# Kernel tuning notes

Measured on AMD Instinct MI355X. Metric: run time of the kernel, lower is better.

The kernel has to match this reference:

```python
import jax, jax.numpy as jnp
import numpy as np

EMBED_DIM = 1024
NUM_HEADS = 8
SEQ_LEN = 2048
EPS = 1e-6


def setup_inputs() -> dict:
    key = jax.random.key(0)
    ks = jax.random.split(key, 8)
    E, NH, S = EMBED_DIM, NUM_HEADS, SEQ_LEN
    q = jax.random.normal(ks[0], (S, E), jnp.float32)
    k = jax.random.normal(ks[1], (S, E), jnp.float32)
    v = jax.random.normal(ks[2], (S, E), jnp.float32)
    # gate projections: weights init'd to zeros in the module; use small random
    # values so the gate math is exercised. Biases follow the module's init.
    Wi = 0.02 * jax.random.normal(ks[3], (NH, 3 * E), jnp.float32)
    bi = jnp.linspace(3.0, 6.0, NH, dtype=jnp.float32)
    Wf = 0.02 * jax.random.normal(ks[4], (NH, 3 * E), jnp.float32)
    bf = jnp.sqrt(0.1) * jax.random.normal(ks[5], (NH,), jnp.float32)
    # ResidualLayerNorm (xLSTM-style): effective scale = 1 + weight, no bias
    ln_weight = jnp.zeros((E,), jnp.float32)
    return {"q": q, "k": k, "v": v, "Wi": Wi, "bi": bi, "Wf": Wf, "bf": bf,
            "ln_weight": ln_weight}


def _mlstm_parallel(q, k, v, Wi, bi, Wf, bf, ln_weight):
    S, E = q.shape
    NH = Wi.shape[0]
    DH = E // NH
    gate_in = jnp.concatenate((q, k, v), axis=1)            # (S, 3E)
    ig = (gate_in @ Wi.T + bi).T[:, :, None]                # (NH, S, 1)
    fg = (gate_in @ Wf.T + bf).T[:, :, None]                # (NH, S, 1)

    qh = q.reshape(S, NH, DH).transpose(1, 0, 2)            # (NH, S, DH)
    kh = k.reshape(S, NH, DH).transpose(1, 0, 2)
    vh = v.reshape(S, NH, DH).transpose(1, 0, 2)

    # cumulative log forget gates
    log_f = jax.nn.log_sigmoid(fg)                          # (NH, S, 1)
    log_f_cum = jnp.concatenate(
        [jnp.zeros((NH, 1, 1), q.dtype), jnp.cumsum(log_f, axis=1)], axis=1
    )                                                       # (NH, S+1, 1)
    log_fg_mat = log_f_cum - log_f_cum.transpose(0, 2, 1)   # (NH, S+1, S+1)
    causal = jnp.tril(jnp.ones((S, S), bool))
    log_fg_mat = jnp.where(causal, log_fg_mat[:, 1:, 1:], -jnp.inf)  # (NH,S,S)

    log_D = log_fg_mat + ig.transpose(0, 2, 1)              # (NH, S, S)
    max_log_D = jnp.max(log_D, axis=-1, keepdims=True)      # (NH, S, 1)
    D = jnp.exp(log_D - max_log_D)                          # stabilized

    qk = jnp.einsum('hsd,htd->hst', qh, kh) / jnp.sqrt(jnp.asarray(DH, q.dtype))
    C = qk * D                                              # (NH, S, S)
    normalizer = jnp.maximum(jnp.abs(jnp.sum(C, axis=-1, keepdims=True)),
                             jnp.exp(-max_log_D))
    C_norm = C / (normalizer + EPS)
    h = jnp.einsum('hst,htd->hsd', C_norm, vh)              # (NH, S, DH)
    h = h.transpose(1, 0, 2).reshape(S, E)

    # residual layer norm: LN(h) * (1 + weight), no bias
    mu = jnp.mean(h, axis=-1, keepdims=True)
    var = jnp.mean(jnp.square(h - mu), axis=-1, keepdims=True)
    h_norm = (h - mu) * jax.lax.rsqrt(var + 1e-5)
    return h_norm * (1.0 + ln_weight)


def reference(q, k, v, Wi, bi, Wf, bf, ln_weight):
    return _mlstm_parallel(q, k, v, Wi, bi, Wf, bf, ln_weight)
```

## Files before the change

kernel.cpp:

```cpp
#include <hip/hip_runtime.h>
#include <math.h>

#define S_LEN 2048
#define EMB   1024
#define NHEAD 8
#define DH    128
#define E3    3072
#define BM    64
#define BN    32
#define NSPLIT 4
#define KSTRIDE  136
#define VTSTRIDE 40
#define PTSTRIDE 40

typedef __bf16 bf16x8 __attribute__((ext_vector_type(8)));
typedef __bf16 bf16x4 __attribute__((ext_vector_type(4)));
typedef float  f32x4  __attribute__((ext_vector_type(4)));

__global__ __launch_bounds__(256) void gates_cvt_transpose_kernel(
    const float* __restrict__ q, const float* __restrict__ k,
    const float* __restrict__ v,
    const float* __restrict__ Wi, const float* __restrict__ bi,
    const float* __restrict__ Wf, const float* __restrict__ bf,
    __bf16* __restrict__ Qh, __bf16* __restrict__ Ql,
    __bf16* __restrict__ Kh, __bf16* __restrict__ Kl,
    __bf16* __restrict__ Vt,
    float* __restrict__ ig, float* __restrict__ lf)
{
    const int tid = threadIdx.x;
    __shared__ union {
        float red[16][4];
        __bf16 tile[32][33];
    } sh;

    if (blockIdx.x < S_LEN) {
        const int t = blockIdx.x;
        const float4 qv = ((const float4*)q)[(size_t)t * 256 + tid];
        const float4 kv = ((const float4*)k)[(size_t)t * 256 + tid];
        const float4 vv = ((const float4*)v)[(size_t)t * 256 + tid];
        {
            size_t idx = (size_t)t * 256 + tid;
            bf16x4 hi, lo;
            hi[0]=(__bf16)qv.x; hi[1]=(__bf16)qv.y; hi[2]=(__bf16)qv.z; hi[3]=(__bf16)qv.w;
            lo[0]=(__bf16)(qv.x-(float)hi[0]); lo[1]=(__bf16)(qv.y-(float)hi[1]);
            lo[2]=(__bf16)(qv.z-(float)hi[2]); lo[3]=(__bf16)(qv.w-(float)hi[3]);
            ((bf16x4*)Qh)[idx] = hi; ((bf16x4*)Ql)[idx] = lo;
            hi[0]=(__bf16)kv.x; hi[1]=(__bf16)kv.y; hi[2]=(__bf16)kv.z; hi[3]=(__bf16)kv.w;
            lo[0]=(__bf16)(kv.x-(float)hi[0]); lo[1]=(__bf16)(kv.y-(float)hi[1]);
            lo[2]=(__bf16)(kv.z-(float)hi[2]); lo[3]=(__bf16)(kv.w-(float)hi[3]);
            ((bf16x4*)Kh)[idx] = hi; ((bf16x4*)Kl)[idx] = lo;
        }
        float acc[16];
        #pragma unroll
        for (int g = 0; g < 16; ++g) {
            const float4* w4 = (const float4*)((g < 8) ? (Wi + g * E3) : (Wf + (g - 8) * E3));
            float4 a = w4[tid], b = w4[256 + tid], c = w4[512 + tid];
            acc[g] = a.x*qv.x + a.y*qv.y + a.z*qv.z + a.w*qv.w
                   + b.x*kv.x + b.y*kv.y + b.z*kv.z + b.w*kv.w
                   + c.x*vv.x + c.y*vv.y + c.z*vv.z + c.w*vv.w;
        }
        const int w = tid >> 6, lane = tid & 63;
        #pragma unroll
        for (int g = 0; g < 16; ++g) {
            float x = acc[g];
            for (int o = 32; o > 0; o >>= 1) x += __shfl_down(x, o, 64);
            if (lane == 0) sh.red[g][w] = x;
        }
        __syncthreads();
        if (tid < 16) {
            float s = sh.red[tid][0] + sh.red[tid][1] + sh.red[tid][2] + sh.red[tid][3];
            if (tid < 8) {
                ig[tid * S_LEN + t] = s + bi[tid];
            } else {
                int h = tid - 8;
                float x = s + bf[h];
                lf[h * S_LEN + t] = fminf(x, 0.f) - log1pf(expf(-fabsf(x)));
            }
        }
    } else {
        const int tb = blockIdx.x - S_LEN;
        const int sb = (tb & 63) * 32, eb = (tb >> 6) * 32;
        #pragma unroll
        for (int i = 0; i < 4; ++i) {
            int lin = tid + i * 256;
            int sr = lin >> 5, ec = lin & 31;
            sh.tile[ec][sr] = (__bf16)v[(size_t)(sb + sr) * EMB + eb + ec];
        }
        __syncthreads();
        #pragma unroll
        for (int i = 0; i < 4; ++i) {
            int lin = tid + i * 256;
            int er = lin >> 5, sc = lin & 31;
            Vt[(size_t)(eb + er) * S_LEN + sb + sc] = sh.tile[er][sc];
        }
    }
}

__global__ __launch_bounds__(256) void cumsum_aux_kernel(
    const float* __restrict__ lf, const float* __restrict__ ig,
    float* __restrict__ F, float* __restrict__ ug,
    float* __restrict__ umax, float* __restrict__ upmax)
{
    const int h = blockIdx.x, tid = threadIdx.x;
    __shared__ float ssum[256];
    __shared__ float morig[256];
    float loc[8];
    const int base = tid * 8;
    float s = 0.f;
    for (int i = 0; i < 8; i++) { s += lf[h * S_LEN + base + i]; loc[i] = s; }
    ssum[tid] = s;
    __syncthreads();
    for (int o = 1; o < 256; o <<= 1) {
        float add = (tid >= o) ? ssum[tid - o] : 0.f;
        __syncthreads();
        ssum[tid] += add;
        __syncthreads();
    }
    float prev = (tid > 0) ? ssum[tid - 1] : 0.f;
    float* Fh = F + h * (S_LEN + 1);
    if (tid == 0) Fh[0] = 0.f;
    float Fv[8];
    for (int i = 0; i < 8; i++) { Fv[i] = prev + loc[i]; Fh[base + i + 1] = Fv[i]; }

    const float* igh = ig + h * S_LEN;
    float pm[8];
    float runm = -1e30f;
    #pragma unroll
    for (int i = 0; i < 8; i++) {
        float u = igh[base + i] - Fv[i];
        ug[h * S_LEN + base + i] = u;
        runm = fmaxf(runm, u);
        pm[i] = runm;
    }
    morig[tid] = runm;
    __syncthreads();
    const int g0 = tid & ~3;
    float pfx = -1e30f;
    for (int j = g0; j < tid; ++j) pfx = fmaxf(pfx, morig[j]);
    #pragma unroll
    for (int i = 0; i < 8; i++)
        upmax[h * S_LEN + base + i] = fmaxf(pfx, pm[i]);
    if ((tid & 3) == 0) {
        float mm = fmaxf(fmaxf(morig[tid], morig[tid + 1]),
                         fmaxf(morig[tid + 2], morig[tid + 3]));
        umax[h * 64 + (tid >> 2)] = mm;
    }
}

__global__ __launch_bounds__(256, 2) void mlstm_mfma(
    const __bf16* __restrict__ Qhg, const __bf16* __restrict__ Qlg,
    const __bf16* __restrict__ Khg, const __bf16* __restrict__ Klg,
    const __bf16* __restrict__ Vtg,
    const float* __restrict__ ug, const float* __restrict__ umaxg,
    const float* __restrict__ upmaxg, const float* __restrict__ F,
    __bf16* __restrict__ Opart, float* __restrict__ msplit,
    float* __restrict__ lsplit)
{
    const int flat = blockIdx.x;
    const int h = flat & 7;
    const int rest = flat >> 3;
    const int xx = rest & 15, z = rest >> 4;
    const int tid  = threadIdx.x;
    const int lane = tid & 63, w = tid >> 6;
    const int quad = lane >> 4, l15 = lane & 15;

    __shared__ __bf16 Kh[BN * KSTRIDE], Kl[BN * KSTRIDE];
    __shared__ __bf16 Vt[DH * VTSTRIDE];
    __shared__ __bf16 Pt[4][16 * PTSTRIDE];

    const float* Fh  = F  + h * (S_LEN + 1);
    const float* ugh = ug + h * S_LEN;
    const float scale = 0.088388347648318447f;
    const int kr  = tid >> 4, kc8 = tid & 15;
    const int vr0 = tid >> 2, vc0 = tid & 3;

    for (int pair = 0; pair < 2; ++pair) {
        const int qt = (pair == 0) ? xx : 31 - xx;
        const int qb = qt * BM;
        const int nj = 2 * qt + 2;
        const int j0 = (z * nj) / NSPLIT, j1 = ((z + 1) * nj) / NSPLIT;

        float fq[4], upm[4];
        int sglob[4], sblk[4];
        #pragma unroll
        for (int r = 0; r < 4; ++r) {
            int s = qb + w * 16 + quad * 4 + r;
            sglob[r] = s; sblk[r] = s >> 5;
            fq[r]  = Fh[s + 1];
            upm[r] = upmaxg[h * S_LEN + s];
        }
        float m_r[4] = {-1e30f, -1e30f, -1e30f, -1e30f};
        float l_r[4] = {0.f, 0.f, 0.f, 0.f};
        f32x4 Oacc[8] = {{0,0,0,0},{0,0,0,0},{0,0,0,0},{0,0,0,0},
                         {0,0,0,0},{0,0,0,0},{0,0,0,0},{0,0,0,0}};

        bf16x8 pk[2], pl[2], pv[2];
        if (j0 < j1) {
            const int tb = j0 * BN;
            #pragma unroll
            for (int i = 0; i < 2; ++i) {
                int row = kr + 16 * i;
                size_t g = (size_t)(tb + row) * EMB + h * DH + kc8 * 8;
                pk[i] = *(const bf16x8*)(Khg + g);
                pl[i] = *(const bf16x8*)(Klg + g);
                pv[i] = *(const bf16x8*)(Vtg + (size_t)(h * DH + vr0 + 64 * i) * S_LEN + tb + vc0 * 8);
            }
        }

        for (int j = j0; j < j1; ++j) {
            const int tb = j * BN;
            __syncthreads();
            #pragma unroll
            for (int i = 0; i < 2; ++i) {
                int row = kr + 16 * i;
                *(bf16x8*)&Kh[row * KSTRIDE + kc8 * 8] = pk[i];
                *(bf16x8*)&Kl[row * KSTRIDE + kc8 * 8] = pl[i];
                *(bf16x8*)&Vt[(vr0 + 64 * i) * VTSTRIDE + vc0 * 8] = pv[i];
            }
            __syncthreads();
            if (j + 1 < j1) {
                const int tb2 = tb + BN;
                #pragma unroll
                for (int i = 0; i < 2; ++i) {
                    int row = kr + 16 * i;
                    size_t g = (size_t)(tb2 + row) * EMB + h * DH + kc8 * 8;
                    pk[i] = *(const bf16x8*)(Khg + g);
                    pl[i] = *(const bf16x8*)(Klg + g);
                    pv[i] = *(const bf16x8*)(Vtg + (size_t)(h * DH + vr0 + 64 * i) * S_LEN + tb2 + vc0 * 8);
                }
            }
            bf16x8 qh[4], ql[4];
            {
                const size_t qrow = (size_t)(qb + w * 16 + l15) * EMB + h * DH + quad * 8;
                #pragma unroll
                for (int kk = 0; kk < 4; ++kk) {
                    qh[kk] = *(const bf16x8*)(Qhg + qrow + kk * 32);
                    ql[kk] = *(const bf16x8*)(Qlg + qrow + kk * 32);
                }
            }
            f32x4 S0 = {0,0,0,0}, S1 = {0,0,0,0};
            #pragma unroll
            for (int kk = 0; kk < 4; ++kk) {
                const int co = kk * 32 + quad * 8;
                bf16x8 bh0 = *(const bf16x8*)&Kh[l15 * KSTRIDE + co];
                bf16x8 bl0 = *(const bf16x8*)&Kl[l15 * KSTRIDE + co];
                S0 = __builtin_amdgcn_mfma_f32_16x16x32_bf16(qh[kk], bh0, S0, 0, 0, 0);
                S0 = __builtin_amdgcn_mfma_f32_16x16x32_bf16(qh[kk], bl0, S0, 0, 0, 0);
                S0 = __builtin_amdgcn_mfma_f32_16x16x32_bf16(ql[kk], bh0, S0, 0, 0, 0);
                bf16x8 bh1 = *(const bf16x8*)&Kh[(16 + l15) * KSTRIDE + co];
                bf16x8 bl1 = *(const bf16x8*)&Kl[(16 + l15) * KSTRIDE + co];
                S1 = __builtin_amdgcn_mfma_f32_16x16x32_bf16(qh[kk], bh1, S1, 0, 0, 0);
                S1 = __builtin_amdgcn_mfma_f32_16x16x32_bf16(qh[kk], bl1, S1, 0, 0, 0);
                S1 = __builtin_amdgcn_mfma_f32_16x16x32_bf16(ql[kk], bh1, S1, 0, 0, 0);
            }
            const int t0 = tb + l15, t1 = tb + 16 + l15;
            const float ut0 = ugh[t0], ut1 = ugh[t1];
            const float umj = umaxg[h * 64 + j];
            #pragma unroll
            for (int r = 0; r < 4; ++r) {
                float mt = (j < sblk[r]) ? (fq[r] + umj)
                         : (j == sblk[r]) ? (fq[r] + upm[r]) : -1e30f;
                float mn = fmaxf(m_r[r], mt);
                float alpha = __expf(m_r[r] - mn);
                m_r[r] = mn;
                l_r[r] *= alpha;
                #pragma unroll
                for (int nt = 0; nt < 8; ++nt) Oacc[nt][r] *= alpha;
                float p0 = __expf(fq[r] + ut0 - mn) * S0[r] * scale;
                float p1 = __expf(fq[r] + ut1 - mn) * S1[r] * scale;
                if (j >= sblk[r]) {
                    if (t0 > sglob[r]) p0 = 0.f;
                    if (t1 > sglob[r]) p1 = 0.f;
                }
                float x = p0 + p1;
                #pragma unroll
                for (int o = 1; o < 16; o <<= 1) x += __shfl_xor(x, o);
                l_r[r] += x;
                const int prow = (quad * 4 + r) * PTSTRIDE;
                Pt[w][prow + l15]      = (__bf16)p0;
                Pt[w][prow + 16 + l15] = (__bf16)p1;
            }
            bf16x8 pa = *(const bf16x8*)&Pt[w][l15 * PTSTRIDE + quad * 8];
            #pragma unroll
            for (int nt = 0; nt < 8; ++nt) {
                bf16x8 vb = *(const bf16x8*)&Vt[(nt * 16 + l15) * VTSTRIDE + quad * 8];
                Oacc[nt] = __builtin_amdgcn_mfma_f32_16x16x32_bf16(pa, vb, Oacc[nt], 0, 0, 0);
            }
        }
        __bf16* Oz = Opart + (size_t)z * S_LEN * EMB;
        #pragma unroll
        for (int nt = 0; nt < 8; ++nt) {
            #pragma unroll
            for (int r = 0; r < 4; ++r) {
                Oz[(size_t)sglob[r] * EMB + h * DH + nt * 16 + l15] = (__bf16)Oacc[nt][r];
            }
        }
        if (l15 == 0) {
            #pragma unroll
            for (int r = 0; r < 4; ++r) {
                msplit[(z * NHEAD + h) * S_LEN + sglob[r]] = m_r[r];
                lsplit[(z * NHEAD + h) * S_LEN + sglob[r]] = l_r[r];
            }
        }
    }
}

__global__ __launch_bounds__(256) void combine_ln_kernel(
    const __bf16* __restrict__ Opart, const float* __restrict__ msplit,
    const float* __restrict__ lsplit, const float* __restrict__ lnw,
    float* __restrict__ out)
{
    const int tid = threadIdx.x;
    const int r  = tid >> 7;
    const int wr = (tid >> 6) & 1;
    const int c0 = (tid & 127) * 8;
    const int hh = c0 >> 7;
    const int s  = blockIdx.x * 2 + r;
    __shared__ float redsum[2][2], redvar[2][2];

    float m = -1e30f, es[NSPLIT], l = 0.f;
    #pragma unroll
    for (int zz = 0; zz < NSPLIT; ++zz)
        m = fmaxf(m, msplit[(zz * NHEAD + hh) * S_LEN + s]);
    #pragma unroll
    for (int zz = 0; zz < NSPLIT; ++zz) {
        es[zz] = __expf(msplit[(zz * NHEAD + hh) * S_LEN + s] - m);
        l += es[zz] * lsplit[(zz * NHEAD + hh) * S_LEN + s];
    }
    const float rn = 1.f / (fmaxf(fabsf(l), __expf(-m)) + 1e-6f);

    const size_t SE = (size_t)S_LEN * EMB;
    float x[8] = {0,0,0,0,0,0,0,0};
    #pragma unroll
    for (int zz = 0; zz < NSPLIT; ++zz) {
        bf16x8 o = *(const bf16x8*)(Opart + zz * SE + (size_t)s * EMB + c0);
        #pragma unroll
        for (int e = 0; e < 8; ++e) x[e] += es[zz] * (float)o[e];
    }
    float sum = 0.f;
    #pragma unroll
    for (int e = 0; e < 8; ++e) { x[e] *= rn; sum += x[e]; }
    for (int o = 32; o > 0; o >>= 1) sum += __shfl_down(sum, o, 64);
    if ((tid & 63) == 0) redsum[r][wr] = sum;
    __syncthreads();
    sum = redsum[r][0] + redsum[r][1];
    const float mu = sum * (1.f / EMB);
    float vs = 0.f;
    #pragma unroll
    for (int e = 0; e < 8; ++e) { float d = x[e] - mu; vs += d * d; }
    for (int o = 32; o > 0; o >>= 1) vs += __shfl_down(vs, o, 64);
    if ((tid & 63) == 0) redvar[r][wr] = vs;
    __syncthreads();
    vs = redvar[r][0] + redvar[r][1];
    const float rstd = rsqrtf(vs * (1.f / EMB) + 1e-5f);
    const float4 w0 = *(const float4*)(lnw + c0);
    const float4 w1 = *(const float4*)(lnw + c0 + 4);
    float4 o0, o1;
    o0.x = (x[0]-mu)*rstd*(1.f+w0.x); o0.y = (x[1]-mu)*rstd*(1.f+w0.y);
    o0.z = (x[2]-mu)*rstd*(1.f+w0.z); o0.w = (x[3]-mu)*rstd*(1.f+w0.w);
    o1.x = (x[4]-mu)*rstd*(1.f+w1.x); o1.y = (x[5]-mu)*rstd*(1.f+w1.y);
    o1.z = (x[6]-mu)*rstd*(1.f+w1.z); o1.w = (x[7]-mu)*rstd*(1.f+w1.w);
    *(float4*)(out + (size_t)s * EMB + c0)     = o0;
    *(float4*)(out + (size_t)s * EMB + c0 + 4) = o1;
}

extern "C" void kernel_launch(void* const* d_in, const int* in_sizes, int n_in,
                              void* d_out, int out_size, void* d_ws, size_t ws_size,
                              hipStream_t stream)
{
    const float* q   = (const float*)d_in[0];
    const float* k   = (const float*)d_in[1];
    const float* v   = (const float*)d_in[2];
    const float* Wi  = (const float*)d_in[3];
    const float* bi  = (const float*)d_in[4];
    const float* Wf  = (const float*)d_in[5];
    const float* bf  = (const float*)d_in[6];
    const float* lnw = (const float*)d_in[7];
    float* out = (float*)d_out;

    float* ws = (float*)d_ws;
    float* ig    = ws;
    float* lf    = ig + NHEAD * S_LEN;
    float* F     = lf + NHEAD * S_LEN;
    float* ugw   = F + NHEAD * (S_LEN + 1);
    float* umaxw = ugw + NHEAD * S_LEN;
    float* upmaxw= umaxw + NHEAD * 64;
    __bf16* Qh = (__bf16*)(upmaxw + NHEAD * S_LEN);
    const size_t SEb = (size_t)S_LEN * EMB;
    __bf16* Ql  = Qh + SEb;
    __bf16* Kh  = Ql + SEb;
    __bf16* Kl  = Kh + SEb;
    __bf16* Vtg = Kl + SEb;
    __bf16* Opart = Vtg + SEb;
    float* msplit = (float*)(Opart + (size_t)NSPLIT * SEb);
    float* lsplit = msplit + NSPLIT * NHEAD * S_LEN;

    gates_cvt_transpose_kernel<<<2 * S_LEN, 256, 0, stream>>>(
        q, k, v, Wi, bi, Wf, bf, Qh, Ql, Kh, Kl, Vtg, ig, lf);
    cumsum_aux_kernel<<<NHEAD, 256, 0, stream>>>(lf, ig, F, ugw, umaxw, upmaxw);
    mlstm_mfma<<<16 * NHEAD * NSPLIT, 256, 0, stream>>>(
        Qh, Ql, Kh, Kl, Vtg, ugw, umaxw, upmaxw, F, Opart, msplit, lsplit);
    combine_ln_kernel<<<S_LEN / 2, 256, 0, stream>>>(Opart, msplit, lsplit, lnw, out);
}
```

Baseline: 160.5 us.

## Split paired query tiles into separate blocks, hoist Q loads, skip masked tiles

Each block now handles a single query tile instead of a (qt, 31-qt) pair, which doubles the grid and alternates forward and reverse tile order by split index for load balance. The Q fragments are loaded once before the key loop instead of on every iteration. The per-tile gate values are prefetched alongside K/V. Fully masked key tiles are skipped per wave. The row-sum shuffle reduction moves out of the loop into a single reduction at the end. The added blocks raise launch count, and the per-wave skip leaves the block-level syncs in place.

```diff
diff --git a/kernel.cpp b/kernel.cpp
--- a/kernel.cpp
+++ b/kernel.cpp
@@ -156,10 +156,13 @@
     __bf16* __restrict__ Opart, float* __restrict__ msplit,
     float* __restrict__ lsplit)
 {
-    const int flat = blockIdx.x;
-    const int h = flat & 7;
-    const int rest = flat >> 3;
-    const int xx = rest & 15, z = rest >> 4;
+    const int flat  = blockIdx.x;
+    const int chunk = flat >> 8;
+    const int m8    = flat & 255;
+    const int h     = m8 & 7;
+    const int e     = m8 >> 3;
+    const int qt    = (chunk & 1) ? (31 - e) : e;
+    const int z     = chunk;
     const int tid  = threadIdx.x;
     const int lane = tid & 63, w = tid >> 6;
     const int quad = lane >> 4, l15 = lane & 15;
@@ -174,70 +177,79 @@
     const int kr  = tid >> 4, kc8 = tid & 15;
     const int vr0 = tid >> 2, vc0 = tid & 3;
 
-    for (int pair = 0; pair < 2; ++pair) {
-        const int qt = (pair == 0) ? xx : 31 - xx;
-        const int qb = qt * BM;
-        const int nj = 2 * qt + 2;
-        const int j0 = (z * nj) / NSPLIT, j1 = ((z + 1) * nj) / NSPLIT;
-
-        float fq[4], upm[4];
-        int sglob[4], sblk[4];
-        #pragma unroll
-        for (int r = 0; r < 4; ++r) {
-            int s = qb + w * 16 + quad * 4 + r;
-            sglob[r] = s; sblk[r] = s >> 5;
-            fq[r]  = Fh[s + 1];
-            upm[r] = upmaxg[h * S_LEN + s];
-        }
-        float m_r[4] = {-1e30f, -1e30f, -1e30f, -1e30f};
-        float l_r[4] = {0.f, 0.f, 0.f, 0.f};
-        f32x4 Oacc[8] = {{0,0,0,0},{0,0,0,0},{0,0,0,0},{0,0,0,0},
-                         {0,0,0,0},{0,0,0,0},{0,0,0,0},{0,0,0,0}};
-
-        bf16x8 pk[2], pl[2], pv[2];
-        if (j0 < j1) {
-            const int tb = j0 * BN;
+    const int qb  = qt * BM;
+    const int nj  = 2 * qt + 2;
+    const int j0  = (z * nj) / NSPLIT, j1 = ((z + 1) * nj) / NSPLIT;
+    const int qbw = qb + w * 16;
+    const int SBLK = (qb >> 5) + (w >> 1);
+
+    float fq[4], upm[4];
+    #pragma unroll
+    for (int r = 0; r < 4; ++r) {
+        int s = qbw + quad * 4 + r;
+        fq[r]  = Fh[s + 1];
+        upm[r] = upmaxg[h * S_LEN + s];
+    }
+
+    bf16x8 qh[4], ql[4];
+    {
+        const size_t qrow = (size_t)(qbw + l15) * EMB + h * DH + quad * 8;
+        #pragma unroll
+        for (int kk = 0; kk < 4; ++kk) {
+            qh[kk] = *(const bf16x8*)(Qhg + qrow + kk * 32);
+            ql[kk] = *(const bf16x8*)(Qlg + qrow + kk * 32);
+        }
+    }
+
+    float m_r[4] = {-1e30f, -1e30f, -1e30f, -1e30f};
+    float l_r[4] = {0.f, 0.f, 0.f, 0.f};
+    f32x4 Oacc[8] = {{0,0,0,0},{0,0,0,0},{0,0,0,0},{0,0,0,0},
+                     {0,0,0,0},{0,0,0,0},{0,0,0,0},{0,0,0,0}};
+
+    bf16x8 pk[2], pl[2], pv[2];
+    float pu0 = 0.f, pu1 = 0.f, pum = 0.f;
+    if (j0 < j1) {
+        const int tb = j0 * BN;
+        #pragma unroll
+        for (int i = 0; i < 2; ++i) {
+            int row = kr + 16 * i;
+            size_t g = (size_t)(tb + row) * EMB + h * DH + kc8 * 8;
+            pk[i] = *(const bf16x8*)(Khg + g);
+            pl[i] = *(const bf16x8*)(Klg + g);
+            pv[i] = *(const bf16x8*)(Vtg + (size_t)(h * DH + vr0 + 64 * i) * S_LEN + tb + vc0 * 8);
+        }
+        pu0 = ugh[tb + l15];
+        pu1 = ugh[tb + 16 + l15];
+        pum = umaxg[h * 64 + j0];
+    }
+
+    for (int j = j0; j < j1; ++j) {
+        const int tb = j * BN;
+        __syncthreads();
+        #pragma unroll
+        for (int i = 0; i < 2; ++i) {
+            int row = kr + 16 * i;
+            *(bf16x8*)&Kh[row * KSTRIDE + kc8 * 8] = pk[i];
+            *(bf16x8*)&Kl[row * KSTRIDE + kc8 * 8] = pl[i];
+            *(bf16x8*)&Vt[(vr0 + 64 * i) * VTSTRIDE + vc0 * 8] = pv[i];
+        }
+        __syncthreads();
+        const float ut0 = pu0, ut1 = pu1, umj = pum;
+        if (j + 1 < j1) {
+            const int tb2 = tb + BN;
             #pragma unroll
             for (int i = 0; i < 2; ++i) {
                 int row = kr + 16 * i;
-                size_t g = (size_t)(tb + row) * EMB + h * DH + kc8 * 8;
+                size_t g = (size_t)(tb2 + row) * EMB + h * DH + kc8 * 8;
                 pk[i] = *(const bf16x8*)(Khg + g);
                 pl[i] = *(const bf16x8*)(Klg + g);
-                pv[i] = *(const bf16x8*)(Vtg + (size_t)(h * DH + vr0 + 64 * i) * S_LEN + tb + vc0 * 8);
+                pv[i] = *(const bf16x8*)(Vtg + (size_t)(h * DH + vr0 + 64 * i) * S_LEN + tb2 + vc0 * 8);
             }
-        }
-
-        for (int j = j0; j < j1; ++j) {
-            const int tb = j * BN;
-            __syncthreads();
-            #pragma unroll
-            for (int i = 0; i < 2; ++i) {
-                int row = kr + 16 * i;
-                *(bf16x8*)&Kh[row * KSTRIDE + kc8 * 8] = pk[i];
-                *(bf16x8*)&Kl[row * KSTRIDE + kc8 * 8] = pl[i];
-                *(bf16x8*)&Vt[(vr0 + 64 * i) * VTSTRIDE + vc0 * 8] = pv[i];
-            }
-            __syncthreads();
-            if (j + 1 < j1) {
-                const int tb2 = tb + BN;
-                #pragma unroll
-                for (int i = 0; i < 2; ++i) {
-                    int row = kr + 16 * i;
-                    size_t g = (size_t)(tb2 + row) * EMB + h * DH + kc8 * 8;
-                    pk[i] = *(const bf16x8*)(Khg + g);
-                    pl[i] = *(const bf16x8*)(Klg + g);
-                    pv[i] = *(const bf16x8*)(Vtg + (size_t)(h * DH + vr0 + 64 * i) * S_LEN + tb2 + vc0 * 8);
-                }
-            }
-            bf16x8 qh[4], ql[4];
-            {
-                const size_t qrow = (size_t)(qb + w * 16 + l15) * EMB + h * DH + quad * 8;
-                #pragma unroll
-                for (int kk = 0; kk < 4; ++kk) {
-                    qh[kk] = *(const bf16x8*)(Qhg + qrow + kk * 32);
-                    ql[kk] = *(const bf16x8*)(Qlg + qrow + kk * 32);
-                }
-            }
+            pu0 = ugh[tb2 + l15];
+            pu1 = ugh[tb2 + 16 + l15];
+            pum = umaxg[h * 64 + (j + 1)];
+        }
+        if (j <= SBLK) {
             f32x4 S0 = {0,0,0,0}, S1 = {0,0,0,0};
             #pragma unroll
             for (int kk = 0; kk < 4; ++kk) {
@@ -254,28 +266,22 @@
                 S1 = __builtin_amdgcn_mfma_f32_16x16x32_bf16(ql[kk], bh1, S1, 0, 0, 0);
             }
             const int t0 = tb + l15, t1 = tb + 16 + l15;
-            const float ut0 = ugh[t0], ut1 = ugh[t1];
-            const float umj = umaxg[h * 64 + j];
             #pragma unroll
             for (int r = 0; r < 4; ++r) {
-                float mt = (j < sblk[r]) ? (fq[r] + umj)
-                         : (j == sblk[r]) ? (fq[r] + upm[r]) : -1e30f;
+                float mt = (j < SBLK) ? (fq[r] + umj) : (fq[r] + upm[r]);
                 float mn = fmaxf(m_r[r], mt);
                 float alpha = __expf(m_r[r] - mn);
                 m_r[r] = mn;
-                l_r[r] *= alpha;
                 #pragma unroll
                 for (int nt = 0; nt < 8; ++nt) Oacc[nt][r] *= alpha;
                 float p0 = __expf(fq[r] + ut0 - mn) * S0[r] * scale;
                 float p1 = __expf(fq[r] + ut1 - mn) * S1[r] * scale;
-                if (j >= sblk[r]) {
-                    if (t0 > sglob[r]) p0 = 0.f;
-                    if (t1 > sglob[r]) p1 = 0.f;
+                if (j == SBLK) {
+                    int sg = qbw + quad * 4 + r;
+                    if (t0 > sg) p0 = 0.f;
+                    if (t1 > sg) p1 = 0.f;
                 }
-                float x = p0 + p1;
-                #pragma unroll
-                for (int o = 1; o < 16; o <<= 1) x += __shfl_xor(x, o);
-                l_r[r] += x;
+                l_r[r] = l_r[r] * alpha + (p0 + p1);
                 const int prow = (quad * 4 + r) * PTSTRIDE;
                 Pt[w][prow + l15]      = (__bf16)p0;
                 Pt[w][prow + 16 + l15] = (__bf16)p1;
@@ -287,20 +293,29 @@
                 Oacc[nt] = __builtin_amdgcn_mfma_f32_16x16x32_bf16(pa, vb, Oacc[nt], 0, 0, 0);
             }
         }
-        __bf16* Oz = Opart + (size_t)z * S_LEN * EMB;
-        #pragma unroll
-        for (int nt = 0; nt < 8; ++nt) {
-            #pragma unroll
-            for (int r = 0; r < 4; ++r) {
-                Oz[(size_t)sglob[r] * EMB + h * DH + nt * 16 + l15] = (__bf16)Oacc[nt][r];
-            }
-        }
-        if (l15 == 0) {
-            #pragma unroll
-            for (int r = 0; r < 4; ++r) {
-                msplit[(z * NHEAD + h) * S_LEN + sglob[r]] = m_r[r];
-                lsplit[(z * NHEAD + h) * S_LEN + sglob[r]] = l_r[r];
-            }
+    }
+    __bf16* Oz = Opart + (size_t)z * S_LEN * EMB;
+    #pragma unroll
+    for (int nt = 0; nt < 8; ++nt) {
+        #pragma unroll
+        for (int r = 0; r < 4; ++r) {
+            int sg = qbw + quad * 4 + r;
+            Oz[(size_t)sg * EMB + h * DH + nt * 16 + l15] = (__bf16)Oacc[nt][r];
+        }
+    }
+    #pragma unroll
+    for (int r = 0; r < 4; ++r) {
+        float x = l_r[r];
+        #pragma unroll
+        for (int o = 1; o < 16; o <<= 1) x += __shfl_xor(x, o);
+        l_r[r] = x;
+    }
+    if (l15 == 0) {
+        #pragma unroll
+        for (int r = 0; r < 4; ++r) {
+            int sg = qbw + quad * 4 + r;
+            msplit[(z * NHEAD + h) * S_LEN + sg] = m_r[r];
+            lsplit[(z * NHEAD + h) * S_LEN + sg] = l_r[r];
         }
     }
 }
@@ -398,7 +413,7 @@
     gates_cvt_transpose_kernel<<<2 * S_LEN, 256, 0, stream>>>(
         q, k, v, Wi, bi, Wf, bf, Qh, Ql, Kh, Kl, Vtg, ig, lf);
     cumsum_aux_kernel<<<NHEAD, 256, 0, stream>>>(lf, ig, F, ugw, umaxw, upmaxw);
-    mlstm_mfma<<<16 * NHEAD * NSPLIT, 256, 0, stream>>>(
+    mlstm_mfma<<<32 * NHEAD * NSPLIT, 256, 0, stream>>>(
         Qh, Ql, Kh, Kl, Vtg, ugw, umaxw, upmaxw, F, Opart, msplit, lsplit);
     combine_ln_kernel<<<S_LEN / 2, 256, 0, stream>>>(Opart, msplit, lsplit, lnw, out);
 }
```

Result: no change. 162.8 us (+1.5%).

## Skip fully masked tiles, hoist Q loads, defer row-sum reduction, warp-shuffle scan

Applied to the files above, without the earlier changes.

The attention loop now skips QK and PV work for key blocks lying entirely above the causal diagonal of each wave's 16 rows, which the old code computed and then masked to zero. Q fragments are loaded once per query tile instead of once per key block. The gate values ug and umax are prefetched one iteration ahead, and the per-row sum shuffle reduction moves out of the loop into a single pass at the end. The cumsum kernel's shared-memory Hillis-Steele scan is replaced by a wave shuffle scan plus a 4-entry cross-wave combine. Keeping Q resident adds register pressure, and the per-wave branch around the MFMA work makes waves in a block diverge.

```diff
diff --git a/kernel.cpp b/kernel.cpp
--- a/kernel.cpp
+++ b/kernel.cpp
@@ -102,21 +102,25 @@
     float* __restrict__ umax, float* __restrict__ upmax)
 {
     const int h = blockIdx.x, tid = threadIdx.x;
-    __shared__ float ssum[256];
+    const int lane = tid & 63, w = tid >> 6;
+    __shared__ float wsum[4];
     __shared__ float morig[256];
     float loc[8];
     const int base = tid * 8;
     float s = 0.f;
     for (int i = 0; i < 8; i++) { s += lf[h * S_LEN + base + i]; loc[i] = s; }
-    ssum[tid] = s;
+    float inc = s;
+    #pragma unroll
+    for (int o = 1; o < 64; o <<= 1) {
+        float t = __shfl_up(inc, o, 64);
+        if (lane >= o) inc += t;
+    }
+    if (lane == 63) wsum[w] = inc;
     __syncthreads();
-    for (int o = 1; o < 256; o <<= 1) {
-        float add = (tid >= o) ? ssum[tid - o] : 0.f;
-        __syncthreads();
-        ssum[tid] += add;
-        __syncthreads();
-    }
-    float prev = (tid > 0) ? ssum[tid - 1] : 0.f;
+    float wpre = 0.f;
+    #pragma unroll
+    for (int i = 0; i < 4; ++i) if (i < w) wpre += wsum[i];
+    const float prev = wpre + inc - s;
     float* Fh = F + h * (S_LEN + 1);
     if (tid == 0) Fh[0] = 0.f;
     float Fv[8];
@@ -179,22 +183,39 @@
         const int qb = qt * BM;
         const int nj = 2 * qt + 2;
         const int j0 = (z * nj) / NSPLIT, j1 = ((z + 1) * nj) / NSPLIT;
+        const int qbw = qb + w * 16;
+        const int SBLK = (qb >> 5) + (w >> 1);
 
         float fq[4], upm[4];
-        int sglob[4], sblk[4];
+        int sglob[4];
         #pragma unroll
         for (int r = 0; r < 4; ++r) {
-            int s = qb + w * 16 + quad * 4 + r;
-            sglob[r] = s; sblk[r] = s >> 5;
+            int s = qbw + quad * 4 + r;
+            sglob[r] = s;
             fq[r]  = Fh[s + 1];
             upm[r] = upmaxg[h * S_LEN + s];
         }
+
+        bf16x8 qh[4], ql[4];
+        {
+            const size_t qrow = (size_t)(qbw + l15) * EMB + h * DH + quad * 8;
+            #pragma unroll
+            for (int kk = 0; kk < 4; ++kk) {
+                qh[kk] = *(const bf16x8*)(Qhg + qrow + kk * 32);
+                ql[kk] = *(const bf16x8*)(Qlg + qrow + kk * 32);
+            }
+        }
+        #pragma unroll
+        for (int kk = 0; kk < 4; ++kk)
+            asm volatile("" : "+v"(qh[kk]), "+v"(ql[kk]));
+
         float m_r[4] = {-1e30f, -1e30f, -1e30f, -1e30f};
         float l_r[4] = {0.f, 0.f, 0.f, 0.f};
         f32x4 Oacc[8] = {{0,0,0,0},{0,0,0,0},{0,0,0,0},{0,0,0,0},
                          {0,0,0,0},{0,0,0,0},{0,0,0,0},{0,0,0,0}};
 
         bf16x8 pk[2], pl[2], pv[2];
+        float pu0 = 0.f, pu1 = 0.f, pum = 0.f;
         if (j0 < j1) {
             const int tb = j0 * BN;
             #pragma unroll
@@ -205,6 +226,9 @@
                 pl[i] = *(const bf16x8*)(Klg + g);
                 pv[i] = *(const bf16x8*)(Vtg + (size_t)(h * DH + vr0 + 64 * i) * S_LEN + tb + vc0 * 8);
             }
+            pu0 = ugh[tb + l15];
+            pu1 = ugh[tb + 16 + l15];
+            pum = umaxg[h * 64 + j0];
         }
 
         for (int j = j0; j < j1; ++j) {
@@ -218,6 +242,7 @@
                 *(bf16x8*)&Vt[(vr0 + 64 * i) * VTSTRIDE + vc0 * 8] = pv[i];
             }
             __syncthreads();
+            const float ut0 = pu0, ut1 = pu1, umj = pum;
             if (j + 1 < j1) {
                 const int tb2 = tb + BN;
                 #pragma unroll
@@ -228,63 +253,52 @@
                     pl[i] = *(const bf16x8*)(Klg + g);
                     pv[i] = *(const bf16x8*)(Vtg + (size_t)(h * DH + vr0 + 64 * i) * S_LEN + tb2 + vc0 * 8);
                 }
-            }
-            bf16x8 qh[4], ql[4];
-            {
-                const size_t qrow = (size_t)(qb + w * 16 + l15) * EMB + h * DH + quad * 8;
+                pu0 = ugh[tb2 + l15];
+                pu1 = ugh[tb2 + 16 + l15];
+                pum = umaxg[h * 64 + (j + 1)];
+            }
+            if (j <= SBLK) {
+                f32x4 S0 = {0,0,0,0}, S1 = {0,0,0,0};
                 #pragma unroll
                 for (int kk = 0; kk < 4; ++kk) {
-                    qh[kk] = *(const bf16x8*)(Qhg + qrow + kk * 32);
-                    ql[kk] = *(const bf16x8*)(Qlg + qrow + kk * 32);
+                    const int co = kk * 32 + quad * 8;
+                    bf16x8 bh0 = *(const bf16x8*)&Kh[l15 * KSTRIDE + co];
+                    bf16x8 bl0 = *(const bf16x8*)&Kl[l15 * KSTRIDE + co];
+                    S0 = __builtin_amdgcn_mfma_f32_16x16x32_bf16(qh[kk], bh0, S0, 0, 0, 0);
+                    S0 = __builtin_amdgcn_mfma_f32_16x16x32_bf16(qh[kk], bl0, S0, 0, 0, 0);
+                    S0 = __builtin_amdgcn_mfma_f32_16x16x32_bf16(ql[kk], bh0, S0, 0, 0, 0);
+                    bf16x8 bh1 = *(const bf16x8*)&Kh[(16 + l15) * KSTRIDE + co];
+                    bf16x8 bl1 = *(const bf16x8*)&Kl[(16 + l15) * KSTRIDE + co];
+                    S1 = __builtin_amdgcn_mfma_f32_16x16x32_bf16(qh[kk], bh1, S1, 0, 0, 0);
+                    S1 = __builtin_amdgcn_mfma_f32_16x16x32_bf16(qh[kk], bl1, S1, 0, 0, 0);
+                    S1 = __builtin_amdgcn_mfma_f32_16x16x32_bf16(ql[kk], bh1, S1, 0, 0, 0);
                 }
-            }
-            f32x4 S0 = {0,0,0,0}, S1 = {0,0,0,0};
-            #pragma unroll
-            for (int kk = 0; kk < 4; ++kk) {
-                const int co = kk * 32 + quad * 8;
-                bf16x8 bh0 = *(const bf16x8*)&Kh[l15 * KSTRIDE + co];
-                bf16x8 bl0 = *(const bf16x8*)&Kl[l15 * KSTRIDE + co];
-                S0 = __builtin_amdgcn_mfma_f32_16x16x32_bf16(qh[kk], bh0, S0, 0, 0, 0);
-                S0 = __builtin_amdgcn_mfma_f32_16x16x32_bf16(qh[kk], bl0, S0, 0, 0, 0);
-                S0 = __builtin_amdgcn_mfma_f32_16x16x32_bf16(ql[kk], bh0, S0, 0, 0, 0);
-                bf16x8 bh1 = *(const bf16x8*)&Kh[(16 + l15) * KSTRIDE + co];
-                bf16x8 bl1 = *(const bf16x8*)&Kl[(16 + l15) * KSTRIDE + co];
-                S1 = __builtin_amdgcn_mfma_f32_16x16x32_bf16(qh[kk], bh1, S1, 0, 0, 0);
-                S1 = __builtin_amdgcn_mfma_f32_16x16x32_bf16(qh[kk], bl1, S1, 0, 0, 0);
-                S1 = __builtin_amdgcn_mfma_f32_16x16x32_bf16(ql[kk], bh1, S1, 0, 0, 0);
-            }
-            const int t0 = tb + l15, t1 = tb + 16 + l15;
-            const float ut0 = ugh[t0], ut1 = ugh[t1];
-            const float umj = umaxg[h * 64 + j];
-            #pragma unroll
-            for (int r = 0; r < 4; ++r) {
-                float mt = (j < sblk[r]) ? (fq[r] + umj)
-                         : (j == sblk[r]) ? (fq[r] + upm[r]) : -1e30f;
-                float mn = fmaxf(m_r[r], mt);
-                float alpha = __expf(m_r[r] - mn);
-                m_r[r] = mn;
-                l_r[r] *= alpha;
+                const int t0 = tb + l15, t1 = tb + 16 + l15;
                 #pragma unroll
-                for (int nt = 0; nt < 8; ++nt) Oacc[nt][r] *= alpha;
-                float p0 = __expf(fq[r] + ut0 - mn) * S0[r] * scale;
-                float p1 = __expf(fq[r] + ut1 - mn) * S1[r] * scale;
-                if (j >= sblk[r]) {
-                    if (t0 > sglob[r]) p0 = 0.f;
-                    if (t1 > sglob[r]) p1 = 0.f;
+                for (int r = 0; r < 4; ++r) {
+                    float mt = (j < SBLK) ? (fq[r] + umj) : (fq[r] + upm[r]);
+                    float mn = fmaxf(m_r[r], mt);
+                    float alpha = __expf(m_r[r] - mn);
+                    m_r[r] = mn;
+                    #pragma unroll
+                    for (int nt = 0; nt < 8; ++nt) Oacc[nt][r] *= alpha;
+                    float p0 = __expf(fq[r] + ut0 - mn) * S0[r] * scale;
+                    float p1 = __expf(fq[r] + ut1 - mn) * S1[r] * scale;
+                    if (j == SBLK) {
+                        if (t0 > sglob[r]) p0 = 0.f;
+                        if (t1 > sglob[r]) p1 = 0.f;
+                    }
+                    l_r[r] = l_r[r] * alpha + (p0 + p1);
+                    const int prow = (quad * 4 + r) * PTSTRIDE;
+                    Pt[w][prow + l15]      = (__bf16)p0;
+                    Pt[w][prow + 16 + l15] = (__bf16)p1;
                 }
-                float x = p0 + p1;
+                bf16x8 pa = *(const bf16x8*)&Pt[w][l15 * PTSTRIDE + quad * 8];
                 #pragma unroll
-                for (int o = 1; o < 16; o <<= 1) x += __shfl_xor(x, o);
-                l_r[r] += x;
-                const int prow = (quad * 4 + r) * PTSTRIDE;
-                Pt[w][prow + l15]      = (__bf16)p0;
-                Pt[w][prow + 16 + l15] = (__bf16)p1;
-            }
-            bf16x8 pa = *(const bf16x8*)&Pt[w][l15 * PTSTRIDE + quad * 8];
-            #pragma unroll
-            for (int nt = 0; nt < 8; ++nt) {
-                bf16x8 vb = *(const bf16x8*)&Vt[(nt * 16 + l15) * VTSTRIDE + quad * 8];
-                Oacc[nt] = __builtin_amdgcn_mfma_f32_16x16x32_bf16(pa, vb, Oacc[nt], 0, 0, 0);
+                for (int nt = 0; nt < 8; ++nt) {
+                    bf16x8 vb = *(const bf16x8*)&Vt[(nt * 16 + l15) * VTSTRIDE + quad * 8];
+                    Oacc[nt] = __builtin_amdgcn_mfma_f32_16x16x32_bf16(pa, vb, Oacc[nt], 0, 0, 0);
+                }
             }
         }
         __bf16* Oz = Opart + (size_t)z * S_LEN * EMB;
@@ -294,6 +308,13 @@
             for (int r = 0; r < 4; ++r) {
                 Oz[(size_t)sglob[r] * EMB + h * DH + nt * 16 + l15] = (__bf16)Oacc[nt][r];
             }
+        }
+        #pragma unroll
+        for (int r = 0; r < 4; ++r) {
+            float x = l_r[r];
+            #pragma unroll
+            for (int o = 1; o < 16; o <<= 1) x += __shfl_xor(x, o);
+            l_r[r] = x;
         }
         if (l15 == 0) {
             #pragma unroll
```

New measurement: 157.5 us. No clear change (-1.9%).
